# Kernel optimization log

Measured on AMD Instinct MI355X. Metric: run time of the kernel, lower is better.

## Reference

```python
import jax, jax.numpy as jnp
import numpy as np

B, L, IDIM = 2, 4096, 2048
N_HEADS, N_GROUPS, HEAD_DIM = 16, 4, 128
GROUP_SIZE = N_HEADS // N_GROUPS
WINDOW = 1024
SCALE = 256.0 ** -0.5  # query_pre_attn_scalar = 256
EPS = 1e-6


def setup_inputs() -> dict:
    key = jax.random.key(0)
    ks = jax.random.split(key, 8)
    x = jax.random.normal(ks[0], (B, L, IDIM), dtype=jnp.float32)
    # realistic RoPE tables
    inv_freq = 1.0 / (10000.0 ** (np.arange(0, HEAD_DIM, 2, dtype=np.float32) / HEAD_DIM))
    t = np.arange(L, dtype=np.float32)
    freqs = np.outer(t, inv_freq)                      # [L, HEAD_DIM//2]
    emb = np.concatenate([freqs, freqs], axis=-1)      # [L, HEAD_DIM]
    cos = jnp.asarray(np.cos(emb), dtype=jnp.float32)
    sin = jnp.asarray(np.sin(emb), dtype=jnp.float32)
    s = 0.02
    Wq = jax.random.normal(ks[1], (IDIM, N_HEADS * HEAD_DIM), dtype=jnp.float32) * s
    Wk = jax.random.normal(ks[2], (IDIM, N_GROUPS * HEAD_DIM), dtype=jnp.float32) * s
    Wv = jax.random.normal(ks[3], (IDIM, N_GROUPS * HEAD_DIM), dtype=jnp.float32) * s
    Wo = jax.random.normal(ks[4], (N_HEADS * HEAD_DIM, IDIM), dtype=jnp.float32) * s
    qn_w = jnp.ones((HEAD_DIM,), dtype=jnp.float32)
    kn_w = jnp.ones((HEAD_DIM,), dtype=jnp.float32)
    return {"x": x, "cos": cos, "sin": sin, "Wq": Wq, "Wk": Wk, "Wv": Wv, "Wo": Wo, "qn_w": qn_w, "kn_w": kn_w}


def _rmsnorm(x, w):
    var = jnp.mean(jnp.square(x), axis=-1, keepdims=True)
    return x * jax.lax.rsqrt(var + EPS) * w


def _rope(x, cos, sin):
    # x: [b, h, l, d]; cos/sin: [l, d]
    d2 = x.shape[-1] // 2
    x1, x2 = x[..., :d2], x[..., d2:]
    rot = jnp.concatenate([-x2, x1], axis=-1)
    return x * cos[None, None] + rot * sin[None, None]


def reference(x, cos, sin, Wq, Wk, Wv, Wo, qn_w, kn_w):
    b, l, _ = x.shape
    q = (x @ Wq).reshape(b, l, N_HEADS, HEAD_DIM).transpose(0, 2, 1, 3)   # b h l d
    k = (x @ Wk).reshape(b, l, N_GROUPS, HEAD_DIM).transpose(0, 2, 1, 3)  # b g l d
    v = (x @ Wv).reshape(b, l, N_GROUPS, HEAD_DIM).transpose(0, 2, 1, 3)  # b g l d
    q = _rmsnorm(q, qn_w)
    k = _rmsnorm(k, kn_w)
    q = _rope(q, cos, sin)
    k = _rope(k, cos, sin)
    k = jnp.repeat(k, GROUP_SIZE, axis=1)  # b h l d
    v = jnp.repeat(v, GROUP_SIZE, axis=1)
    dots = jnp.einsum('bhid,bhjd->bhij', q, k) * SCALE
    i = jnp.arange(l)[:, None]
    j = jnp.arange(l)[None, :]
    allowed = (j <= i) & (j > i - WINDOW)  # causal sliding window
    dots = jnp.where(allowed[None, None], dots, -jnp.inf)
    attn = jax.nn.softmax(dots, axis=-1)
    out = jnp.einsum('bhij,bhjd->bhid', attn, v)
    out = out.transpose(0, 2, 1, 3).reshape(b, l, N_HEADS * HEAD_DIM)
    return out @ Wo
```

## Files before the change

kernel.cpp:

```cpp
#include <hip/hip_runtime.h>
#include <hip/hip_bf16.h>

typedef __hip_bfloat16 bf16;
typedef __attribute__((ext_vector_type(8))) __bf16 bf16x8;
typedef __attribute__((ext_vector_type(4))) float f32x4;

#define MFMA16(a, b, c) __builtin_amdgcn_mfma_f32_16x16x32_bf16((a), (b), (c), 0, 0, 0)

static __device__ __forceinline__ void gload_lds16(const void* g, void* l) {
    typedef const __attribute__((address_space(1))) unsigned gq_t;
    typedef __attribute__((address_space(3))) unsigned ls_t;
    __builtin_amdgcn_global_load_lds((gq_t*)g, (ls_t*)l, 16, 0, 0);
}

static __device__ __forceinline__ unsigned short f2bfbits(float f) {
    bf16 h = __float2bfloat16(f);
    return *reinterpret_cast<unsigned short*>(&h);
}

__global__ __launch_bounds__(256) void cvt_bf16_kernel(const float* __restrict__ in,
                                                       bf16* __restrict__ out, int n) {
    int i = (blockIdx.x * 256 + threadIdx.x) * 8;
    if (i < n) {
        float4 a = *reinterpret_cast<const float4*>(in + i);
        float4 b = *reinterpret_cast<const float4*>(in + i + 4);
        bf16 tmp[8];
        tmp[0] = __float2bfloat16(a.x); tmp[1] = __float2bfloat16(a.y);
        tmp[2] = __float2bfloat16(a.z); tmp[3] = __float2bfloat16(a.w);
        tmp[4] = __float2bfloat16(b.x); tmp[5] = __float2bfloat16(b.y);
        tmp[6] = __float2bfloat16(b.z); tmp[7] = __float2bfloat16(b.w);
        *reinterpret_cast<uint4*>(out + i) = *reinterpret_cast<const uint4*>(tmp);
    }
}

__global__ __launch_bounds__(256) void transpose_wqkv_kernel(const float* __restrict__ Wq,
                                                             const float* __restrict__ Wk,
                                                             const float* __restrict__ Wv,
                                                             bf16* __restrict__ out) {
    __shared__ float tile[32][33];
    int k0 = blockIdx.x * 32;
    int n0 = blockIdx.y * 32;
    int tx = threadIdx.x & 31, ty = threadIdx.x >> 5;
#pragma unroll
    for (int i = 0; i < 4; ++i) {
        int k = k0 + ty + i * 8, n = n0 + tx;
        float v;
        if (n < 2048)      v = Wq[(size_t)k * 2048 + n];
        else if (n < 2560) v = Wk[(size_t)k * 512 + (n - 2048)];
        else               v = Wv[(size_t)k * 512 + (n - 2560)];
        tile[ty + i * 8][tx] = v;
    }
    __syncthreads();
#pragma unroll
    for (int i = 0; i < 4; ++i)
        out[(size_t)(n0 + ty + i * 8) * 2048 + k0 + tx] = __float2bfloat16(tile[tx][ty + i * 8]);
}

__global__ __launch_bounds__(256) void transpose_w_kernel(const float* __restrict__ in,
                                                          bf16* __restrict__ out) {
    __shared__ float tile[32][33];
    int k0 = blockIdx.x * 32, n0 = blockIdx.y * 32;
    int tx = threadIdx.x & 31, ty = threadIdx.x >> 5;
#pragma unroll
    for (int i = 0; i < 4; ++i)
        tile[ty + i * 8][tx] = in[(size_t)(k0 + ty + i * 8) * 2048 + n0 + tx];
    __syncthreads();
#pragma unroll
    for (int i = 0; i < 4; ++i)
        out[(size_t)(n0 + ty + i * 8) * 2048 + k0 + tx] = __float2bfloat16(tile[tx][ty + i * 8]);
}

template <int NFRAG, bool OUT_F32>
__global__ __launch_bounds__(512, 2) void gemm8p_kernel(const bf16* __restrict__ A,
                                                        const bf16* __restrict__ BT,
                                                        void* __restrict__ Cv,
                                                        int M, int N, int K, int nbn) {
    constexpr int BN = NFRAG * 64;
    constexpr int PB = NFRAG;
    __shared__ bf16 As[2][256 * 64];
    __shared__ bf16 Bs[2][BN * 64];
    int t = threadIdx.x;
    int lane = t & 63, w = t >> 6;
    int wm = w >> 2, wn = w & 3;
    int lr = lane & 15, lq = lane >> 4;
    int lin = blockIdx.x;
    int cpx = gridDim.x >> 3;
    int wg = (lin & 7) * cpx + (lin >> 3);
    int bm = wg / nbn, bn = wg % nbn;
    const bf16* Ab = A + (size_t)bm * 256 * K;
    const bf16* Bb = BT + (size_t)bn * BN * K;

    auto stA = [&](int slot, int kt, int piece) {
        int idx = piece * 512 + t;
        int r = idx >> 3, c8 = idx & 7;
        gload_lds16(Ab + (size_t)r * K + kt * 64 + ((c8 ^ (r & 7)) * 8), &As[slot][idx * 8]);
    };
    auto stB = [&](int slot, int kt, int piece) {
        int idx = piece * 512 + t;
        int r = idx >> 3, c8 = idx & 7;
        gload_lds16(Bb + (size_t)r * K + kt * 64 + ((c8 ^ (r & 7)) * 8), &Bs[slot][idx * 8]);
    };

    f32x4 acc[8][NFRAG] = {};
    bf16x8 bq[NFRAG][2], af[2][2];

    auto readB = [&](int slot) {
#pragma unroll
        for (int n = 0; n < NFRAG; ++n)
#pragma unroll
            for (int ks = 0; ks < 2; ++ks) {
                int ro = wn * (NFRAG * 16) + n * 16 + lr;
                int ch = (ks * 4 + lq) ^ (ro & 7);
                bq[n][ks] = *reinterpret_cast<const bf16x8*>(&Bs[slot][ro * 64 + ch * 8]);
            }
    };
    auto readA = [&](int mbase, int slot) {
#pragma unroll
        for (int mi = 0; mi < 2; ++mi)
#pragma unroll
            for (int ks = 0; ks < 2; ++ks) {
                int ro = wm * 128 + (mbase + mi) * 16 + lr;
                int ch = (ks * 4 + lq) ^ (ro & 7);
                af[mi][ks] = *reinterpret_cast<const bf16x8*>(&As[slot][ro * 64 + ch * 8]);
            }
    };
    auto mf = [&](int mbase) {
#pragma unroll
        for (int mi = 0; mi < 2; ++mi)
#pragma unroll
            for (int n = 0; n < NFRAG; ++n)
#pragma unroll
                for (int ks = 0; ks < 2; ++ks)
                    acc[mbase + mi][n] = MFMA16(af[mi][ks], bq[n][ks], acc[mbase + mi][n]);
    };

#define GATE_PB()                                                          \
    do {                                                                   \
        if constexpr (NFRAG == 4) asm volatile("s_waitcnt vmcnt(4)" ::: "memory"); \
        else                      asm volatile("s_waitcnt vmcnt(3)" ::: "memory"); \
    } while (0)
#define PHASE_TAIL()                                                       \
    do {                                                                   \
        __builtin_amdgcn_s_barrier();                                      \
        asm volatile("s_waitcnt lgkmcnt(0)" ::: "memory");                 \
    } while (0)
#define MFMA_CLUSTER(mb)                                                   \
    do {                                                                   \
        __builtin_amdgcn_s_setprio(1);                                     \
        mf(mb);                                                            \
        __builtin_amdgcn_s_setprio(0);                                     \
        __builtin_amdgcn_s_barrier();                                      \
    } while (0)

    int nkt = K >> 6;
#pragma unroll
    for (int p = 0; p < 4; ++p) stA(0, 0, p);
#pragma unroll
    for (int p = 0; p < PB; ++p) stB(0, 0, p);
#pragma unroll
    for (int p = 0; p < PB; ++p) stB(1, 1, p);
    GATE_PB();
    __builtin_amdgcn_s_barrier();

    int nI = nkt >> 1;
    for (int I = 0; I < nI; ++I) {
        int T = I << 1;
        bool s2 = (T + 2) < nkt, s3 = (T + 3) < nkt;
        readB(0); readA(0, 0);
#pragma unroll
        for (int p = 0; p < 4; ++p) stA(1, T + 1, p);
        PHASE_TAIL();
        MFMA_CLUSTER(0);
        readA(2, 0);
        if (s2) { stB(0, T + 2, 0); stB(0, T + 2, 1); }
        PHASE_TAIL();
        MFMA_CLUSTER(2);
        readA(4, 0);
        if (s2) {
#pragma unroll
            for (int p = 2; p < PB; ++p) stB(0, T + 2, p);
        }
        PHASE_TAIL();
        MFMA_CLUSTER(4);
        readA(6, 0);
        if (s2) GATE_PB();
        else    asm volatile("s_waitcnt vmcnt(0)" ::: "memory");
        PHASE_TAIL();
        MFMA_CLUSTER(6);
        readB(1); readA(0, 1);
        if (s2) {
#pragma unroll
            for (int p = 0; p < 4; ++p) stA(0, T + 2, p);
        }
        PHASE_TAIL();
        MFMA_CLUSTER(0);
        readA(2, 1);
        if (s3) { stB(1, T + 3, 0); stB(1, T + 3, 1); }
        PHASE_TAIL();
        MFMA_CLUSTER(2);
        readA(4, 1);
        if (s3) {
#pragma unroll
            for (int p = 2; p < PB; ++p) stB(1, T + 3, p);
        }
        PHASE_TAIL();
        MFMA_CLUSTER(4);
        readA(6, 1);
        if (s3) GATE_PB();
        else    asm volatile("s_waitcnt vmcnt(0)" ::: "memory");
        PHASE_TAIL();
        MFMA_CLUSTER(6);
    }
#undef GATE_PB
#undef PHASE_TAIL
#undef MFMA_CLUSTER

#pragma unroll
    for (int m = 0; m < 8; ++m)
#pragma unroll
        for (int n = 0; n < NFRAG; ++n) {
            int row = bm * 256 + wm * 128 + m * 16 + lq * 4;
            int col = bn * BN + wn * (NFRAG * 16) + n * 16 + lr;
#pragma unroll
            for (int j = 0; j < 4; ++j) {
                if (OUT_F32)
                    ((float*)Cv)[(size_t)(row + j) * N + col] = acc[m][n][j];
                else
                    ((bf16*)Cv)[(size_t)(row + j) * N + col] = __float2bfloat16(acc[m][n][j]);
            }
        }
}

__global__ __launch_bounds__(256) void normrope_kernel(const bf16* __restrict__ qkv,
                                                       const float* __restrict__ cosT,
                                                       const float* __restrict__ sinT,
                                                       const float* __restrict__ qnw,
                                                       const float* __restrict__ knw,
                                                       bf16* __restrict__ qh,
                                                       bf16* __restrict__ kh) {
    int t = threadIdx.x;
    int lane = t & 63, wv = t >> 6;
    int blk = blockIdx.x;
    int r = blk / 5;
    int s = (blk % 5) * 4 + wv;
    int b = r >> 12, l = r & 4095;
    int e0 = lane * 2;
    const bf16* src = qkv + (size_t)r * 3072 + s * 128;
    ushort2 xu = *reinterpret_cast<const ushort2*>(src + e0);
    float v0 = __uint_as_float((unsigned)xu.x << 16);
    float v1 = __uint_as_float((unsigned)xu.y << 16);
    float ss = v0 * v0 + v1 * v1;
#pragma unroll
    for (int d = 1; d < 64; d <<= 1) ss += __shfl_xor(ss, d, 64);
    float rn = rsqrtf(ss * (1.0f / 128.0f) + 1e-6f);
    const float* wn = (s < 16) ? qnw : knw;
    float2 wv2 = *reinterpret_cast<const float2*>(wn + e0);
    float xn0 = v0 * rn * wv2.x;
    float xn1 = v1 * rn * wv2.y;
    float xp0 = __shfl_xor(xn0, 32, 64);
    float xp1 = __shfl_xor(xn1, 32, 64);
    float r0 = (lane < 32) ? -xp0 : xp0;
    float r1 = (lane < 32) ? -xp1 : xp1;
    float2 c2 = *reinterpret_cast<const float2*>(cosT + (size_t)l * 128 + e0);
    float2 s2 = *reinterpret_cast<const float2*>(sinT + (size_t)l * 128 + e0);
    float o0 = xn0 * c2.x + r0 * s2.x;
    float o1 = xn1 * c2.y + r1 * s2.y;
    ushort2 ou;
    if (s < 16) {
        const float scl = 0.0625f * 1.44269504088896f;
        ou.x = f2bfbits(o0 * scl);
        ou.y = f2bfbits(o1 * scl);
        bf16* dst = qh + ((size_t)(b * 16 + s) * 4096 + l) * 128;
        *reinterpret_cast<ushort2*>(dst + e0) = ou;
    } else {
        int g = s - 16;
        ou.x = f2bfbits(o0);
        ou.y = f2bfbits(o1);
        int sw = (l & 7) << 3;
        bf16* dst = kh + ((size_t)(b * 4 + g) * 4096 + l) * 128;
        *reinterpret_cast<ushort2*>(dst + (e0 ^ sw)) = ou;
    }
}

__global__ __launch_bounds__(256) void vtrans_kernel(const bf16* __restrict__ qkv,
                                                     bf16* __restrict__ vt) {
    __shared__ bf16 tile[64][132];
    int t = threadIdx.x;
    int l0 = blockIdx.x * 64;
    int bg = blockIdx.y;
    int b = bg >> 2, g = bg & 3;
    const bf16* src = qkv + ((size_t)(b * 4096 + l0)) * 3072 + 2560 + g * 128;
#pragma unroll
    for (int i = 0; i < 4; ++i) {
        int c = i * 256 + t;
        int r = c >> 4, c16 = c & 15;
        uint4 v = *reinterpret_cast<const uint4*>(src + (size_t)r * 3072 + c16 * 8);
        *reinterpret_cast<uint2*>(&tile[r][c16 * 8]) = make_uint2(v.x, v.y);
        *reinterpret_cast<uint2*>(&tile[r][c16 * 8 + 4]) = make_uint2(v.z, v.w);
    }
    __syncthreads();
    bf16* dst = vt + (size_t)bg * 128 * 4096 + l0;
    int cj = t & 63;
    int pos = (cj & 0x23) | ((cj & 16) >> 2) | ((cj & 12) << 1);
#pragma unroll
    for (int dd = 0; dd < 32; ++dd) {
        int d = (t >> 6) * 32 + dd;
        dst[(size_t)d * 4096 + (pos ^ ((d & 7) << 3))] = tile[cj][d];
    }
}

__global__ __launch_bounds__(512, 2) void attn_kernel(const bf16* __restrict__ qh,
                                                      const bf16* __restrict__ kh,
                                                      const bf16* __restrict__ vt,
                                                      bf16* __restrict__ ao) {
    __shared__ bf16 Ks[2][64 * 128];
    __shared__ bf16 Vs[2][128 * 64];
    int t = threadIdx.x;
    int lane = t & 63, w = t >> 6;
    int lr = lane & 15, lq = lane >> 4;
    int bid = blockIdx.x;
    int bh = (bid & 7) * 4 + (bid >> 7);
    int qs = ((bid >> 3) & 15) * 256;
    int b = bh >> 4, h = bh & 15, g = h >> 2;
    int row0 = qs + w * 32;
    const bf16* qp = qh + ((size_t)(b * 16 + h) * 4096 + row0) * 128;
    const bf16* kp = kh + (size_t)(b * 4 + g) * 4096 * 128;
    const bf16* vp = vt + (size_t)(b * 4 + g) * 128 * 4096;

    bf16x8 aq[2][4];
#pragma unroll
    for (int g2 = 0; g2 < 2; ++g2)
#pragma unroll
        for (int kk = 0; kk < 4; ++kk)
            aq[g2][kk] = *reinterpret_cast<const bf16x8*>(qp + (size_t)(g2 * 16 + lr) * 128 + kk * 32 + lq * 8);

    f32x4 o0[8] = {}, o1[8] = {};
    float lsum0 = 0.f, lsum1 = 0.f;
    int qi0 = row0 + lr, qi1 = row0 + 16 + lr;
    int sA = max(0, row0 - 1023) >> 6;
    int sB = max(0, row0 + 16 - 1023) >> 6;
    int t1w = row0 >> 6;
    int t0w = sA;
    int t0 = max(0, qs - 1023) >> 6;
    int t1 = (qs + 255) >> 6;

    auto stage = [&](int buf, int kt) {
        int j0 = kt * 64;
        const bf16* kg = kp + (size_t)j0 * 128;
#pragma unroll
        for (int i = 0; i < 2; ++i) {
            int c = i * 512 + t;
            gload_lds16(kg + c * 8, &Ks[buf][c * 8]);
        }
#pragma unroll
        for (int i = 0; i < 2; ++i) {
            int c = i * 512 + t;
            int d = c >> 3, co = (c & 7) * 8;
            gload_lds16(vp + (size_t)d * 4096 + j0 + co, &Vs[buf][c * 8]);
        }
    };

    stage(0, t0);
    int cur = 0;

    for (int kt = t0; kt <= t1; ++kt) {
        if (kt < t1) {
            stage(cur ^ 1, kt + 1);
            asm volatile("s_waitcnt vmcnt(4)" ::: "memory");
        } else {
            asm volatile("s_waitcnt vmcnt(0)" ::: "memory");
        }
        __builtin_amdgcn_s_barrier();
        if (kt >= t0w && kt <= t1w) {
            int j0 = kt * 64;
            f32x4 s0[4] = {}, s1[4] = {};
            __builtin_amdgcn_s_setprio(1);
#pragma unroll
            for (int jt = 0; jt < 4; ++jt) {
                int r = jt * 16 + lr;
                int rs = (r & 7) << 3;
#pragma unroll
                for (int kk = 0; kk < 4; ++kk) {
                    int c = kk * 32 + lq * 8;
                    bf16x8 bk = *reinterpret_cast<const bf16x8*>(&Ks[cur][r * 128 + (c ^ rs)]);
                    s0[jt] = MFMA16(bk, aq[0][kk], s0[jt]);
                    s1[jt] = MFMA16(bk, aq[1][kk], s1[jt]);
                }
            }
            __builtin_amdgcn_s_setprio(0);
            if (kt <= sA + 1 || kt == t1w) {
#pragma unroll
                for (int jt = 0; jt < 4; ++jt)
#pragma unroll
                    for (int j = 0; j < 4; ++j) {
                        int kj = j0 + jt * 16 + lq * 4 + j;
                        if (!(kj <= qi0 && kj > qi0 - 1024)) s0[jt][j] = -1e30f;
                    }
            }
            if (kt <= sB + 1 || kt == t1w) {
#pragma unroll
                for (int jt = 0; jt < 4; ++jt)
#pragma unroll
                    for (int j = 0; j < 4; ++j) {
                        int kj = j0 + jt * 16 + lq * 4 + j;
                        if (!(kj <= qi1 && kj > qi1 - 1024)) s1[jt][j] = -1e30f;
                    }
            }
            unsigned pk0[4][2], pk1[4][2];
#pragma unroll
            for (int jt = 0; jt < 4; ++jt)
#pragma unroll
                for (int hh = 0; hh < 2; ++hh) {
                    float p0 = exp2f(s0[jt][2 * hh] - 11.5415603f);
                    float p1 = exp2f(s0[jt][2 * hh + 1] - 11.5415603f);
                    lsum0 += p0 + p1;
                    asm("v_cvt_pk_bf16_f32 %0, %1, %2" : "=v"(pk0[jt][hh]) : "v"(p0), "v"(p1));
                }
#pragma unroll
            for (int jt = 0; jt < 4; ++jt)
#pragma unroll
                for (int hh = 0; hh < 2; ++hh) {
                    float p0 = exp2f(s1[jt][2 * hh] - 11.5415603f);
                    float p1 = exp2f(s1[jt][2 * hh + 1] - 11.5415603f);
                    lsum1 += p0 + p1;
                    asm("v_cvt_pk_bf16_f32 %0, %1, %2" : "=v"(pk1[jt][hh]) : "v"(p0), "v"(p1));
                }
            __builtin_amdgcn_s_setprio(1);
#pragma unroll
            for (int kk2 = 0; kk2 < 2; ++kk2) {
                union { unsigned u[4]; bf16x8 v; } pu0, pu1;
                pu0.u[0] = pk0[2 * kk2][0]; pu0.u[1] = pk0[2 * kk2][1];
                pu0.u[2] = pk0[2 * kk2 + 1][0]; pu0.u[3] = pk0[2 * kk2 + 1][1];
                pu1.u[0] = pk1[2 * kk2][0]; pu1.u[1] = pk1[2 * kk2][1];
                pu1.u[2] = pk1[2 * kk2 + 1][0]; pu1.u[3] = pk1[2 * kk2 + 1][1];
#pragma unroll
                for (int dt = 0; dt < 8; ++dt) {
                    int r = dt * 16 + lr;
                    int c = kk2 * 32 + lq * 8;
                    bf16x8 bv = *reinterpret_cast<const bf16x8*>(&Vs[cur][r * 64 + (c ^ ((r & 7) << 3))]);
                    o0[dt] = MFMA16(pu0.v, bv, o0[dt]);
                    o1[dt] = MFMA16(pu1.v, bv, o1[dt]);
                }
            }
            __builtin_amdgcn_s_setprio(0);
        }
        __builtin_amdgcn_s_barrier();
        cur ^= 1;
    }
    float lt0 = lsum0, lt1 = lsum1;
    lt0 += __shfl_xor(lt0, 16, 64);  lt0 += __shfl_xor(lt0, 32, 64);
    lt1 += __shfl_xor(lt1, 16, 64);  lt1 += __shfl_xor(lt1, 32, 64);
    float li0 = 1.0f / lt0, li1 = 1.0f / lt1;
    float lv0[4], lv1[4];
#pragma unroll
    for (int j = 0; j < 4; ++j) {
        lv0[j] = __shfl(li0, lq * 4 + j, 64);
        lv1[j] = __shfl(li1, lq * 4 + j, 64);
    }
#pragma unroll
    for (int dt = 0; dt < 8; ++dt)
#pragma unroll
        for (int j = 0; j < 4; ++j) {
            size_t base = (size_t)(b * 4096 + row0 + lq * 4 + j) * 2048 + h * 128 + dt * 16 + lr;
            ao[base] = __float2bfloat16(o0[dt][j] * lv0[j]);
            ao[base + (size_t)16 * 2048] = __float2bfloat16(o1[dt][j] * lv1[j]);
        }
}

extern "C" void kernel_launch(void* const* d_in, const int* in_sizes, int n_in,
                              void* d_out, int out_size, void* d_ws, size_t ws_size,
                              hipStream_t stream) {
    const float* x    = (const float*)d_in[0];
    const float* cosT = (const float*)d_in[1];
    const float* sinT = (const float*)d_in[2];
    const float* Wq   = (const float*)d_in[3];
    const float* Wk   = (const float*)d_in[4];
    const float* Wv   = (const float*)d_in[5];
    const float* Wo   = (const float*)d_in[6];
    const float* qnw  = (const float*)d_in[7];
    const float* knw  = (const float*)d_in[8];

    char* ws = (char*)d_ws;
    bf16* xb    = (bf16*)(ws);
    bf16* wqkvT = (bf16*)(ws + 33554432);
    bf16* woT   = (bf16*)(ws + 46137344);
    bf16* qh    = (bf16*)(ws + 54525952);
    bf16* kh    = (bf16*)(ws + 88080384);
    bf16* vt    = (bf16*)(ws + 96468992);
    bf16* ao    = xb;
    bf16* qkv   = (bf16*)d_out;

    cvt_bf16_kernel<<<8192, 256, 0, stream>>>(x, xb, 16777216);
    transpose_wqkv_kernel<<<dim3(64, 96), 256, 0, stream>>>(Wq, Wk, Wv, wqkvT);
    transpose_w_kernel<<<dim3(64, 64), 256, 0, stream>>>(Wo, woT);
    gemm8p_kernel<3, false><<<512, 512, 0, stream>>>(xb, wqkvT, (void*)qkv, 8192, 3072, 2048, 16);
    normrope_kernel<<<40960, 256, 0, stream>>>(qkv, cosT, sinT, qnw, knw, qh, kh);
    vtrans_kernel<<<dim3(64, 8), 256, 0, stream>>>(qkv, vt);
    attn_kernel<<<512, 512, 0, stream>>>(qh, kh, vt, ao);
    gemm8p_kernel<4, true><<<256, 512, 0, stream>>>(ao, woT, d_out, 8192, 2048, 2048, 8);
}
```

Before: 354.8 us.

## Halve attention block to 4 waves, each computing 64 query rows

The attention kernel now runs 256 threads per block instead of 512. Each wave covers 64 query rows (four 16-row groups) rather than 32, so each V fragment read from LDS feeds four MFMAs and each K fragment feeds two. Q fragments are reloaded from global memory inside the loop instead of being kept in registers, and the staging loops issue twice as many loads per thread. The aim is more LDS reuse per wave and fewer waves contending. The cost is a larger accumulator footprint (32 f32x4 per lane), which adds register pressure and halves the number of waves resident per CU.

```diff
diff --git a/kernel.cpp b/kernel.cpp
--- a/kernel.cpp
+++ b/kernel.cpp
@@ -309,7 +309,7 @@
     }
 }
 
-__global__ __launch_bounds__(512, 2) void attn_kernel(const bf16* __restrict__ qh,
+__global__ __launch_bounds__(256, 2) void attn_kernel(const bf16* __restrict__ qh,
                                                       const bf16* __restrict__ kh,
                                                       const bf16* __restrict__ vt,
                                                       bf16* __restrict__ ao) {
@@ -322,25 +322,16 @@
     int bh = (bid & 7) * 4 + (bid >> 7);
     int qs = ((bid >> 3) & 15) * 256;
     int b = bh >> 4, h = bh & 15, g = h >> 2;
-    int row0 = qs + w * 32;
+    int row0 = qs + w * 64;
     const bf16* qp = qh + ((size_t)(b * 16 + h) * 4096 + row0) * 128;
     const bf16* kp = kh + (size_t)(b * 4 + g) * 4096 * 128;
     const bf16* vp = vt + (size_t)(b * 4 + g) * 128 * 4096;
 
-    bf16x8 aq[2][4];
-#pragma unroll
-    for (int g2 = 0; g2 < 2; ++g2)
-#pragma unroll
-        for (int kk = 0; kk < 4; ++kk)
-            aq[g2][kk] = *reinterpret_cast<const bf16x8*>(qp + (size_t)(g2 * 16 + lr) * 128 + kk * 32 + lq * 8);
-
-    f32x4 o0[8] = {}, o1[8] = {};
-    float lsum0 = 0.f, lsum1 = 0.f;
-    int qi0 = row0 + lr, qi1 = row0 + 16 + lr;
-    int sA = max(0, row0 - 1023) >> 6;
-    int sB = max(0, row0 + 16 - 1023) >> 6;
+    f32x4 o[4][8] = {};
+    float lsum[4] = {0.f, 0.f, 0.f, 0.f};
+    unsigned pk[4][4][2];
+    int t0w = max(0, row0 - 1023) >> 6;
     int t1w = row0 >> 6;
-    int t0w = sA;
     int t0 = max(0, qs - 1023) >> 6;
     int t1 = (qs + 255) >> 6;
 
@@ -348,13 +339,13 @@
         int j0 = kt * 64;
         const bf16* kg = kp + (size_t)j0 * 128;
 #pragma unroll
-        for (int i = 0; i < 2; ++i) {
-            int c = i * 512 + t;
+        for (int i = 0; i < 4; ++i) {
+            int c = i * 256 + t;
             gload_lds16(kg + c * 8, &Ks[buf][c * 8]);
         }
 #pragma unroll
-        for (int i = 0; i < 2; ++i) {
-            int c = i * 512 + t;
+        for (int i = 0; i < 4; ++i) {
+            int c = i * 256 + t;
             int d = c >> 3, co = (c & 7) * 8;
             gload_lds16(vp + (size_t)d * 4096 + j0 + co, &Vs[buf][c * 8]);
         }
@@ -366,80 +357,82 @@
     for (int kt = t0; kt <= t1; ++kt) {
         if (kt < t1) {
             stage(cur ^ 1, kt + 1);
-            asm volatile("s_waitcnt vmcnt(4)" ::: "memory");
+            asm volatile("s_waitcnt vmcnt(8)" ::: "memory");
         } else {
             asm volatile("s_waitcnt vmcnt(0)" ::: "memory");
         }
         __builtin_amdgcn_s_barrier();
         if (kt >= t0w && kt <= t1w) {
             int j0 = kt * 64;
-            f32x4 s0[4] = {}, s1[4] = {};
+            bool mwin = (kt <= t0w + 1);
+            bool mdia = (kt == t1w);
+#pragma unroll
+            for (int pp = 0; pp < 2; ++pp) {
+                f32x4 s0[4] = {}, s1[4] = {};
+                __builtin_amdgcn_s_setprio(1);
+#pragma unroll
+                for (int kk = 0; kk < 4; ++kk) {
+                    bf16x8 qf0 = *reinterpret_cast<const bf16x8*>(
+                        qp + (size_t)((2 * pp) * 16 + lr) * 128 + kk * 32 + lq * 8);
+                    bf16x8 qf1 = *reinterpret_cast<const bf16x8*>(
+                        qp + (size_t)((2 * pp + 1) * 16 + lr) * 128 + kk * 32 + lq * 8);
+#pragma unroll
+                    for (int jt = 0; jt < 4; ++jt) {
+                        int r = jt * 16 + lr;
+                        int c = (kk * 32 + lq * 8) ^ ((r & 7) << 3);
+                        bf16x8 bk = *reinterpret_cast<const bf16x8*>(&Ks[cur][r * 128 + c]);
+                        s0[jt] = MFMA16(bk, qf0, s0[jt]);
+                        s1[jt] = MFMA16(bk, qf1, s1[jt]);
+                    }
+                }
+                __builtin_amdgcn_s_setprio(0);
+                if (mwin || mdia) {
+                    int qi0 = row0 + (2 * pp) * 16 + lr;
+                    int qi1 = row0 + (2 * pp + 1) * 16 + lr;
+#pragma unroll
+                    for (int jt = 0; jt < 4; ++jt)
+#pragma unroll
+                        for (int j = 0; j < 4; ++j) {
+                            int kj = j0 + jt * 16 + lq * 4 + j;
+                            if (!(kj <= qi0 && kj > qi0 - 1024)) s0[jt][j] = -1e30f;
+                            if (!(kj <= qi1 && kj > qi1 - 1024)) s1[jt][j] = -1e30f;
+                        }
+                }
+#pragma unroll
+                for (int jt = 0; jt < 4; ++jt)
+#pragma unroll
+                    for (int hh = 0; hh < 2; ++hh) {
+                        float p0 = exp2f(s0[jt][2 * hh] - 11.5415603f);
+                        float p1 = exp2f(s0[jt][2 * hh + 1] - 11.5415603f);
+                        lsum[2 * pp] += p0 + p1;
+                        asm("v_cvt_pk_bf16_f32 %0, %1, %2"
+                            : "=v"(pk[2 * pp][jt][hh]) : "v"(p0), "v"(p1));
+                        float q0 = exp2f(s1[jt][2 * hh] - 11.5415603f);
+                        float q1 = exp2f(s1[jt][2 * hh + 1] - 11.5415603f);
+                        lsum[2 * pp + 1] += q0 + q1;
+                        asm("v_cvt_pk_bf16_f32 %0, %1, %2"
+                            : "=v"(pk[2 * pp + 1][jt][hh]) : "v"(q0), "v"(q1));
+                    }
+            }
             __builtin_amdgcn_s_setprio(1);
 #pragma unroll
-            for (int jt = 0; jt < 4; ++jt) {
-                int r = jt * 16 + lr;
-                int rs = (r & 7) << 3;
-#pragma unroll
-                for (int kk = 0; kk < 4; ++kk) {
-                    int c = kk * 32 + lq * 8;
-                    bf16x8 bk = *reinterpret_cast<const bf16x8*>(&Ks[cur][r * 128 + (c ^ rs)]);
-                    s0[jt] = MFMA16(bk, aq[0][kk], s0[jt]);
-                    s1[jt] = MFMA16(bk, aq[1][kk], s1[jt]);
+            for (int kk2 = 0; kk2 < 2; ++kk2) {
+                union { unsigned u[4]; bf16x8 v; } pu[4];
+#pragma unroll
+                for (int gg = 0; gg < 4; ++gg) {
+                    pu[gg].u[0] = pk[gg][2 * kk2][0];
+                    pu[gg].u[1] = pk[gg][2 * kk2][1];
+                    pu[gg].u[2] = pk[gg][2 * kk2 + 1][0];
+                    pu[gg].u[3] = pk[gg][2 * kk2 + 1][1];
                 }
-            }
-            __builtin_amdgcn_s_setprio(0);
-            if (kt <= sA + 1 || kt == t1w) {
-#pragma unroll
-                for (int jt = 0; jt < 4; ++jt)
-#pragma unroll
-                    for (int j = 0; j < 4; ++j) {
-                        int kj = j0 + jt * 16 + lq * 4 + j;
-                        if (!(kj <= qi0 && kj > qi0 - 1024)) s0[jt][j] = -1e30f;
-                    }
-            }
-            if (kt <= sB + 1 || kt == t1w) {
-#pragma unroll
-                for (int jt = 0; jt < 4; ++jt)
-#pragma unroll
-                    for (int j = 0; j < 4; ++j) {
-                        int kj = j0 + jt * 16 + lq * 4 + j;
-                        if (!(kj <= qi1 && kj > qi1 - 1024)) s1[jt][j] = -1e30f;
-                    }
-            }
-            unsigned pk0[4][2], pk1[4][2];
-#pragma unroll
-            for (int jt = 0; jt < 4; ++jt)
-#pragma unroll
-                for (int hh = 0; hh < 2; ++hh) {
-                    float p0 = exp2f(s0[jt][2 * hh] - 11.5415603f);
-                    float p1 = exp2f(s0[jt][2 * hh + 1] - 11.5415603f);
-                    lsum0 += p0 + p1;
-                    asm("v_cvt_pk_bf16_f32 %0, %1, %2" : "=v"(pk0[jt][hh]) : "v"(p0), "v"(p1));
-                }
-#pragma unroll
-            for (int jt = 0; jt < 4; ++jt)
-#pragma unroll
-                for (int hh = 0; hh < 2; ++hh) {
-                    float p0 = exp2f(s1[jt][2 * hh] - 11.5415603f);
-                    float p1 = exp2f(s1[jt][2 * hh + 1] - 11.5415603f);
-                    lsum1 += p0 + p1;
-                    asm("v_cvt_pk_bf16_f32 %0, %1, %2" : "=v"(pk1[jt][hh]) : "v"(p0), "v"(p1));
-                }
-            __builtin_amdgcn_s_setprio(1);
-#pragma unroll
-            for (int kk2 = 0; kk2 < 2; ++kk2) {
-                union { unsigned u[4]; bf16x8 v; } pu0, pu1;
-                pu0.u[0] = pk0[2 * kk2][0]; pu0.u[1] = pk0[2 * kk2][1];
-                pu0.u[2] = pk0[2 * kk2 + 1][0]; pu0.u[3] = pk0[2 * kk2 + 1][1];
-                pu1.u[0] = pk1[2 * kk2][0]; pu1.u[1] = pk1[2 * kk2][1];
-                pu1.u[2] = pk1[2 * kk2 + 1][0]; pu1.u[3] = pk1[2 * kk2 + 1][1];
 #pragma unroll
                 for (int dt = 0; dt < 8; ++dt) {
                     int r = dt * 16 + lr;
-                    int c = kk2 * 32 + lq * 8;
-                    bf16x8 bv = *reinterpret_cast<const bf16x8*>(&Vs[cur][r * 64 + (c ^ ((r & 7) << 3))]);
-                    o0[dt] = MFMA16(pu0.v, bv, o0[dt]);
-                    o1[dt] = MFMA16(pu1.v, bv, o1[dt]);
+                    int c = (kk2 * 32 + lq * 8) ^ ((r & 7) << 3);
+                    bf16x8 bv = *reinterpret_cast<const bf16x8*>(&Vs[cur][r * 64 + c]);
+#pragma unroll
+                    for (int gg = 0; gg < 4; ++gg)
+                        o[gg][dt] = MFMA16(pu[gg].v, bv, o[gg][dt]);
                 }
             }
             __builtin_amdgcn_s_setprio(0);
@@ -447,24 +440,24 @@
         __builtin_amdgcn_s_barrier();
         cur ^= 1;
     }
-    float lt0 = lsum0, lt1 = lsum1;
-    lt0 += __shfl_xor(lt0, 16, 64);  lt0 += __shfl_xor(lt0, 32, 64);
-    lt1 += __shfl_xor(lt1, 16, 64);  lt1 += __shfl_xor(lt1, 32, 64);
-    float li0 = 1.0f / lt0, li1 = 1.0f / lt1;
-    float lv0[4], lv1[4];
-#pragma unroll
-    for (int j = 0; j < 4; ++j) {
-        lv0[j] = __shfl(li0, lq * 4 + j, 64);
-        lv1[j] = __shfl(li1, lq * 4 + j, 64);
-    }
-#pragma unroll
-    for (int dt = 0; dt < 8; ++dt)
-#pragma unroll
-        for (int j = 0; j < 4; ++j) {
-            size_t base = (size_t)(b * 4096 + row0 + lq * 4 + j) * 2048 + h * 128 + dt * 16 + lr;
-            ao[base] = __float2bfloat16(o0[dt][j] * lv0[j]);
-            ao[base + (size_t)16 * 2048] = __float2bfloat16(o1[dt][j] * lv1[j]);
-        }
+#pragma unroll
+    for (int gg = 0; gg < 4; ++gg) {
+        float lt = lsum[gg];
+        lt += __shfl_xor(lt, 16, 64);
+        lt += __shfl_xor(lt, 32, 64);
+        float li = 1.0f / lt;
+        float lv[4];
+#pragma unroll
+        for (int j = 0; j < 4; ++j) lv[j] = __shfl(li, lq * 4 + j, 64);
+#pragma unroll
+        for (int dt = 0; dt < 8; ++dt)
+#pragma unroll
+            for (int j = 0; j < 4; ++j) {
+                size_t base = (size_t)(b * 4096 + row0 + gg * 16 + lq * 4 + j) * 2048
+                              + h * 128 + dt * 16 + lr;
+                ao[base] = __float2bfloat16(o[gg][dt][j] * lv[j]);
+            }
+    }
 }
 
 extern "C" void kernel_launch(void* const* d_in, const int* in_sizes, int n_in,
@@ -496,6 +489,6 @@
     gemm8p_kernel<3, false><<<512, 512, 0, stream>>>(xb, wqkvT, (void*)qkv, 8192, 3072, 2048, 16);
     normrope_kernel<<<40960, 256, 0, stream>>>(qkv, cosT, sinT, qnw, knw, qh, kh);
     vtrans_kernel<<<dim3(64, 8), 256, 0, stream>>>(qkv, vt);
-    attn_kernel<<<512, 512, 0, stream>>>(qh, kh, vt, ao);
+    attn_kernel<<<512, 256, 0, stream>>>(qh, kh, vt, ao);
     gemm8p_kernel<4, true><<<256, 512, 0, stream>>>(ao, woT, d_out, 8192, 2048, 2048, 8);
 }
```

New measurement: 474.6 us. 33.8% more time.
